# Kernel optimization log

Measured on AMD Instinct MI355X. Metric: run time of the kernel, lower is better.

The kernel has to match this reference:

```python
import jax, jax.numpy as jnp
import numpy as np

DIM = 512
LEVELS = 4
KSIZES = [3, 5, 7, 9]
NUM_HEADS = 4
GN_GROUPS = 4
GN_EPS = 1e-5
ROPE_BASE = 10000.0


def dwconv(x, w, b):
    # x: (B,C,H,W), w: (C,1,k,k) depthwise, b: (C,)
    y = jax.lax.conv_general_dilated(
        x, w, window_strides=(1, 1), padding='SAME',
        dimension_numbers=('NCHW', 'OIHW', 'NCHW'),
        feature_group_count=x.shape[1])
    return y + b[None, :, None, None]


def groupnorm(x, w, b):
    B, C, H, W = x.shape
    xg = x.reshape(B, GN_GROUPS, C // GN_GROUPS, H, W)
    mu = xg.mean(axis=(2, 3, 4), keepdims=True)
    var = xg.var(axis=(2, 3, 4), keepdims=True)
    xn = ((xg - mu) * jax.lax.rsqrt(var + GN_EPS)).reshape(B, C, H, W)
    return xn * w[None, :, None, None] + b[None, :, None, None]


def rope2d(x):
    # Faithful to the torch RoPE: rotations have shape (h, c//2) and broadcast
    # onto the trailing (w, c//2) dims of x (valid because h == w), so the
    # rotation angle effectively varies along the w axis.
    b, h, w, c = x.shape
    k_max = c // 2
    theta = 1.0 / (ROPE_BASE ** (jnp.arange(k_max, dtype=x.dtype) / k_max))
    angles = jnp.arange(h, dtype=x.dtype)[:, None] * theta[None, :]  # (h, k_max)
    cos = jnp.cos(angles)[None, None, :, :]  # broadcasts along w axis
    sin = jnp.sin(angles)[None, None, :, :]
    xp = x.reshape(b, h, w, k_max, 2)
    re, im = xp[..., 0], xp[..., 1]
    out_re = cos * re - sin * im
    out_im = cos * im + sin * re
    return jnp.stack([out_re, out_im], axis=-1).reshape(b, h, w, c)


def setup_inputs() -> dict:
    key = jax.random.key(0)
    ks = jax.random.split(key, 20)
    C = DIM
    inp = {'x': jax.random.normal(ks[0], (8, C, 64, 64), dtype=jnp.float32)}
    for i, k in enumerate(KSIZES):
        inp[f'conv_w{i}'] = jax.random.normal(ks[1 + i], (C, 1, k, k), dtype=jnp.float32) * 0.05
        inp[f'conv_b{i}'] = jnp.zeros((C,), dtype=jnp.float32)
        inp[f'gn_w{i}'] = jnp.ones((C,), dtype=jnp.float32)
        inp[f'gn_b{i}'] = jnp.zeros((C,), dtype=jnp.float32)
    inp['qk_w'] = jax.random.normal(ks[10], (2 * C, C), dtype=jnp.float32) * (C ** -0.5)
    inp['lepe_w'] = jax.random.normal(ks[11], (C, 1, 3, 3), dtype=jnp.float32) * 0.05
    inp['lepe_b'] = jnp.zeros((C,), dtype=jnp.float32)
    return inp


def reference(x, conv_w0, conv_b0, gn_w0, gn_b0, conv_w1, conv_b1, gn_w1, gn_b1,
              conv_w2, conv_b2, gn_w2, gn_b2, conv_w3, conv_b3, gn_w3, gn_b3,
              qk_w, lepe_w, lepe_b):
    conv_ws = [conv_w0, conv_w1, conv_w2, conv_w3]
    conv_bs = [conv_b0, conv_b1, conv_b2, conv_b3]
    gn_ws = [gn_w0, gn_w1, gn_w2, gn_w3]
    gn_bs = [gn_b0, gn_b1, gn_b2, gn_b3]

    # Multi-level depthwise conv -> GroupNorm -> sigmoid gate, averaged.
    fused = sum(jax.nn.sigmoid(groupnorm(dwconv(x, cw, cb), gw, gb))
                for cw, cb, gw, gb in zip(conv_ws, conv_bs, gn_ws, gn_bs)) / LEVELS

    b, c, h, w = fused.shape
    n = h * w
    H = NUM_HEADS
    hd = c // H

    tokens = fused.transpose(0, 2, 3, 1).reshape(b, n, c)  # (b, n, c)

    qk = tokens @ qk_w.T  # (b, n, 2c)
    q = jax.nn.elu(qk[..., :c]) + 1.0
    k = jax.nn.elu(qk[..., c:]) + 1.0
    v = tokens

    q_rope = rope2d(q.reshape(b, h, w, c)).reshape(b, n, H, hd).transpose(0, 2, 1, 3)
    k_rope = rope2d(k.reshape(b, h, w, c)).reshape(b, n, H, hd).transpose(0, 2, 1, 3)
    qh = q.reshape(b, n, H, hd).transpose(0, 2, 1, 3)  # (b,H,n,hd)
    kh = k.reshape(b, n, H, hd).transpose(0, 2, 1, 3)
    vh = v.reshape(b, n, H, hd).transpose(0, 2, 1, 3)

    k_mean = kh.mean(axis=2, keepdims=True)  # (b,H,1,hd)
    z = 1.0 / (jnp.einsum('bhnd,bhmd->bhnm', qh, k_mean) + 1e-6)  # (b,H,n,1)
    kv = jnp.einsum('bhnd,bhne->bhde', k_rope, vh) / n  # (b,H,hd,hd)
    attn = jnp.einsum('bhnd,bhde->bhne', q_rope, kv) * z  # (b,H,n,hd)

    out_tok = attn.transpose(0, 2, 1, 3).reshape(b, n, c)
    lepe_out = dwconv(fused, lepe_w, lepe_b)  # (b,c,h,w)
    out_tok = out_tok + lepe_out.transpose(0, 2, 3, 1).reshape(b, n, c)

    return out_tok.transpose(0, 2, 1).reshape(b, c, h, w)
```

## Files before the change

kernel.cpp:

```cpp
#include <hip/hip_runtime.h>
#include <math.h>


typedef __attribute__((ext_vector_type(8))) short bf8;
typedef __attribute__((ext_vector_type(4))) float f32x4;

__device__ __forceinline__ float waveSum(float v) {
  #pragma unroll
  for (int o = 32; o; o >>= 1) v += __shfl_down(v, o, 64);
  return v;
}

__device__ __forceinline__ unsigned short f2bf(float f) {
  unsigned u = __float_as_uint(f);
  unsigned r = u + 0x7fffu + ((u >> 16) & 1u);
  return (unsigned short)(r >> 16);
}

__device__ __forceinline__ float bf2f(unsigned short u) {
  return __uint_as_float((unsigned)u << 16);
}

__device__ __forceinline__ void gload_lds16(const void* g, void* l) {
  __builtin_amdgcn_global_load_lds(
      (const __attribute__((address_space(1))) unsigned*)g,
      (__attribute__((address_space(3))) unsigned*)l, 16, 0, 0);
}

__global__ __launch_bounds__(256) void k_ropetab(float* __restrict__ tab) {
  int idx = blockIdx.x * 256 + threadIdx.x;
  int w = idx >> 8, kk = idx & 255;
  float theta = powf(10000.0f, -(float)kk * (1.0f / 256.0f));
  float ang = (float)w * theta;
  tab[2 * idx]     = cosf(ang);
  tab[2 * idx + 1] = sinf(ang);
}

template <int K>
__device__ __forceinline__ void conv8(float (*sm)[73], const float* wl,
                                      int r, int cb, float bias, float acc[8]) {
  constexpr int P = (K - 1) / 2;
  #pragma unroll
  for (int i = 0; i < 8; i++) acc[i] = bias;
  #pragma unroll
  for (int dy = 0; dy < K; ++dy) {
    const float* row = &sm[r + dy - P + 4][cb - P + 4];
    float v[8 + K - 1];
    #pragma unroll
    for (int o = 0; o < 8 + K - 1; ++o) v[o] = row[o];
    #pragma unroll
    for (int dx = 0; dx < K; ++dx) {
      float wv = wl[dy * K + dx];
      #pragma unroll
      for (int i = 0; i < 8; i++) acc[i] = fmaf(wv, v[i + dx], acc[i]);
    }
  }
}

__device__ __forceinline__ void load_plane512(const float* __restrict__ xp,
                                              float (*sm)[73], int tid) {
  for (int idx = tid; idx < 5184; idx += 512) {
    int pr = idx / 72, pc = idx - pr * 72;
    int gr = pr - 4, gc = pc - 4;
    float v = 0.f;
    if ((unsigned)gr < 64u && (unsigned)gc < 64u) v = xp[gr * 64 + gc];
    sm[pr][pc] = v;
  }
}

__device__ __forceinline__ void load_weights512(const float* w0, const float* w1,
                                                const float* w2, const float* w3,
                                                float* wl, int c, int tid) {
  if (tid < 9)               wl[tid]            = w0[c * 9  + tid];
  else if (tid < 34)         wl[tid]            = w1[c * 25 + tid - 9];
  else if (tid < 83)         wl[tid]            = w2[c * 49 + tid - 34];
  else if (tid < 164)        wl[tid]            = w3[c * 81 + tid - 83];
}

__device__ __forceinline__ void reduce_write2_512(float s, float sq, float* red,
                                                  int tid, float* dst) {
  s = waveSum(s); sq = waveSum(sq);
  int wid = tid >> 6, lane = tid & 63;
  if (lane == 0) { red[wid] = s; red[8 + wid] = sq; }
  __syncthreads();
  if (tid == 0) {
    float S = 0.f, SQ = 0.f;
    #pragma unroll
    for (int i = 0; i < 8; i++) { S += red[i]; SQ += red[8 + i]; }
    dst[0] = S; dst[1] = SQ;
  }
  __syncthreads();
}

__global__ __launch_bounds__(512) void k_conv4(
    const float* __restrict__ x,
    const float* __restrict__ w0, const float* __restrict__ b0,
    const float* __restrict__ w1, const float* __restrict__ b1,
    const float* __restrict__ w2, const float* __restrict__ b2,
    const float* __restrict__ w3, const float* __restrict__ b3,
    float* __restrict__ part,
    unsigned short* __restrict__ l0, unsigned short* __restrict__ l1,
    unsigned short* __restrict__ l2, unsigned short* __restrict__ l3) {
  __shared__ float sm[72][73];
  __shared__ float wl[164];
  __shared__ float red[16];
  int tid = threadIdx.x;
  int bc = blockIdx.x;
  int b = bc >> 9, c = bc & 511;
  load_plane512(x + (size_t)bc * 4096, sm, tid);
  load_weights512(w0, w1, w2, w3, wl, c, tid);
  __syncthreads();
  int r = tid >> 3, cb = (tid & 7) << 3;
  size_t obase = (size_t)bc * 4096 + r * 64 + cb;
  float acc[8];
  float s, sq;
  unsigned short o[8];

  conv8<3>(sm, &wl[0], r, cb, b0[c], acc);
  s = 0; sq = 0;
  #pragma unroll
  for (int i = 0; i < 8; i++) {
    s += acc[i]; sq = fmaf(acc[i], acc[i], sq); o[i] = f2bf(acc[i]);
  }
  *(uint4*)&l0[obase] = *(uint4*)&o[0];
  reduce_write2_512(s, sq, red, tid, part + ((size_t)(0 * 8 + b) * 512 + c) * 2);
  __builtin_amdgcn_sched_barrier(0);

  conv8<5>(sm, &wl[9], r, cb, b1[c], acc);
  s = 0; sq = 0;
  #pragma unroll
  for (int i = 0; i < 8; i++) {
    s += acc[i]; sq = fmaf(acc[i], acc[i], sq); o[i] = f2bf(acc[i]);
  }
  *(uint4*)&l1[obase] = *(uint4*)&o[0];
  reduce_write2_512(s, sq, red, tid, part + ((size_t)(1 * 8 + b) * 512 + c) * 2);
  __builtin_amdgcn_sched_barrier(0);

  conv8<7>(sm, &wl[34], r, cb, b2[c], acc);
  s = 0; sq = 0;
  #pragma unroll
  for (int i = 0; i < 8; i++) {
    s += acc[i]; sq = fmaf(acc[i], acc[i], sq); o[i] = f2bf(acc[i]);
  }
  *(uint4*)&l2[obase] = *(uint4*)&o[0];
  reduce_write2_512(s, sq, red, tid, part + ((size_t)(2 * 8 + b) * 512 + c) * 2);
  __builtin_amdgcn_sched_barrier(0);

  conv8<9>(sm, &wl[83], r, cb, b3[c], acc);
  s = 0; sq = 0;
  #pragma unroll
  for (int i = 0; i < 8; i++) {
    s += acc[i]; sq = fmaf(acc[i], acc[i], sq); o[i] = f2bf(acc[i]);
  }
  *(uint4*)&l3[obase] = *(uint4*)&o[0];
  reduce_write2_512(s, sq, red, tid, part + ((size_t)(3 * 8 + b) * 512 + c) * 2);
}

__global__ __launch_bounds__(128) void k_gn_stats(const float* __restrict__ part,
                                                  float* __restrict__ stats) {
  int blk = blockIdx.x;
  int tid = threadIdx.x;
  int g = blk & 3, bb = (blk >> 2) & 7, l = blk >> 5;
  const float* p = part + ((size_t)(l * 8 + bb) * 512 + g * 128 + tid) * 2;
  float s = p[0], sq = p[1];
  s = waveSum(s); sq = waveSum(sq);
  __shared__ float red[4];
  int wid = tid >> 6, lane = tid & 63;
  if (lane == 0) { red[wid] = s; red[2 + wid] = sq; }
  __syncthreads();
  if (tid == 0) {
    float S = red[0] + red[1], SQ = red[2] + red[3];
    const float inv = 1.0f / (128.0f * 4096.0f);
    float mean = S * inv;
    float var = SQ * inv - mean * mean;
    stats[blk * 2] = mean;
    stats[blk * 2 + 1] = rsqrtf(var + 1e-5f);
  }
}

__global__ __launch_bounds__(256) void k_fused_elem(
    const unsigned short* __restrict__ l0, const unsigned short* __restrict__ l1,
    const unsigned short* __restrict__ l2, const unsigned short* __restrict__ l3,
    const float* __restrict__ gw0, const float* __restrict__ gb0,
    const float* __restrict__ gw1, const float* __restrict__ gb1,
    const float* __restrict__ gw2, const float* __restrict__ gb2,
    const float* __restrict__ gw3, const float* __restrict__ gb3,
    const float* __restrict__ stats, float* __restrict__ fused) {
  int bc = blockIdx.x;
  int b = bc >> 9, c = bc & 511, g = c >> 7;
  int tid = threadIdx.x;
  float m0 = stats[(0 * 32 + b * 4 + g) * 2], r0 = stats[(0 * 32 + b * 4 + g) * 2 + 1];
  float m1 = stats[(1 * 32 + b * 4 + g) * 2], r1 = stats[(1 * 32 + b * 4 + g) * 2 + 1];
  float m2 = stats[(2 * 32 + b * 4 + g) * 2], r2 = stats[(2 * 32 + b * 4 + g) * 2 + 1];
  float m3 = stats[(3 * 32 + b * 4 + g) * 2], r3 = stats[(3 * 32 + b * 4 + g) * 2 + 1];
  float a0 = r0 * gw0[c], c0 = gb0[c] - m0 * a0;
  float a1 = r1 * gw1[c], c1 = gb1[c] - m1 * a1;
  float a2 = r2 * gw2[c], c2 = gb2[c] - m2 * a2;
  float a3 = r3 * gw3[c], c3 = gb3[c] - m3 * a3;
  size_t base = (size_t)bc * 4096 + tid * 16;
  uint4 u0a = *(const uint4*)&l0[base], u0b = *(const uint4*)&l0[base + 8];
  uint4 u1a = *(const uint4*)&l1[base], u1b = *(const uint4*)&l1[base + 8];
  uint4 u2a = *(const uint4*)&l2[base], u2b = *(const uint4*)&l2[base + 8];
  uint4 u3a = *(const uint4*)&l3[base], u3b = *(const uint4*)&l3[base + 8];
  float outv[16];
  #pragma unroll
  for (int i = 0; i < 8; i++) {
    float t0 = fmaf(bf2f(((const unsigned short*)&u0a)[i]), a0, c0);
    float t1 = fmaf(bf2f(((const unsigned short*)&u1a)[i]), a1, c1);
    float t2 = fmaf(bf2f(((const unsigned short*)&u2a)[i]), a2, c2);
    float t3 = fmaf(bf2f(((const unsigned short*)&u3a)[i]), a3, c3);
    float s = 1.0f / (1.0f + __expf(-t0)) + 1.0f / (1.0f + __expf(-t1)) +
              1.0f / (1.0f + __expf(-t2)) + 1.0f / (1.0f + __expf(-t3));
    outv[i] = s * 0.25f;
  }
  #pragma unroll
  for (int i = 0; i < 8; i++) {
    float t0 = fmaf(bf2f(((const unsigned short*)&u0b)[i]), a0, c0);
    float t1 = fmaf(bf2f(((const unsigned short*)&u1b)[i]), a1, c1);
    float t2 = fmaf(bf2f(((const unsigned short*)&u2b)[i]), a2, c2);
    float t3 = fmaf(bf2f(((const unsigned short*)&u3b)[i]), a3, c3);
    float s = 1.0f / (1.0f + __expf(-t0)) + 1.0f / (1.0f + __expf(-t1)) +
              1.0f / (1.0f + __expf(-t2)) + 1.0f / (1.0f + __expf(-t3));
    outv[8 + i] = s * 0.25f;
  }
  float* fp = fused + base;
  #pragma unroll
  for (int i = 0; i < 16; i += 4)
    *(float4*)&fp[i] = make_float4(outv[i], outv[i + 1], outv[i + 2], outv[i + 3]);
}

__global__ __launch_bounds__(256) void k_tp(const float* __restrict__ fused,
                                            unsigned short* __restrict__ fbf) {
  __shared__ float sm[64][65];
  int tid = threadIdx.x;
  int bid = blockIdx.x;
  int nt = bid & 63, ct = (bid >> 6) & 7, b = bid >> 9;
  int c0 = ct << 6, n0 = nt << 6;
  int nn = tid & 63, c_s = tid >> 6;
  #pragma unroll
  for (int cc = 0; cc < 64; cc += 4)
    sm[cc + c_s][nn] = fused[((size_t)b * 512 + c0 + cc + c_s) * 4096 + n0 + nn];
  __syncthreads();
  int cc = tid & 63, r_s = tid >> 6;
  #pragma unroll
  for (int r = 0; r < 64; r += 4)
    fbf[((size_t)b * 4096 + n0 + r + r_s) * 512 + c0 + cc] = f2bf(sm[cc][r + r_s]);
}

__global__ __launch_bounds__(256) void k_wcvt(const float* __restrict__ qkw,
                                              unsigned short* __restrict__ wbf) {
  int gid = blockIdx.x * 256 + threadIdx.x;
  float4 v = *(const float4*)&qkw[(size_t)gid * 4];
  short4 o;
  o.x = (short)f2bf(v.x); o.y = (short)f2bf(v.y);
  o.z = (short)f2bf(v.z); o.w = (short)f2bf(v.w);
  *(short4*)&wbf[(size_t)gid * 4] = o;
}

__global__ __launch_bounds__(256) void k_qk(const unsigned short* __restrict__ fbf,
                                            const unsigned short* __restrict__ wbf,
                                            float* __restrict__ qbuf,
                                            float* __restrict__ kbuf) {
  __shared__ __align__(16) short As[8192];
  __shared__ __align__(16) short Bs[8192];
  int tid = threadIdx.x;
  int bid = blockIdx.x;
  int sw = (bid & 7) * 256 + (bid >> 3);
  int b = sw >> 8, rem = sw & 255;
  int mt_blk = rem >> 3, jt = rem & 7;
  int m0 = mt_blk << 7, j0 = jt << 7;
  int lane = tid & 63, wid = tid >> 6;
  int wm = (wid >> 1) * 64, wn = (wid & 1) * 64;
  int l15 = lane & 15, l4 = lane >> 4;

  const unsigned short* Ab = fbf + (size_t)b * 4096 * 512;
  f32x4 acc[4][4];
  #pragma unroll
  for (int i = 0; i < 4; i++)
    #pragma unroll
    for (int j = 0; j < 4; j++) acc[i][j] = (f32x4)0.f;

  int srow[4], sperm[4];
  #pragma unroll
  for (int i = 0; i < 4; i++) {
    int s = i * 256 + tid;
    srow[i] = s >> 3;
    sperm[i] = (s & 7) ^ (srow[i] & 7);
  }

  for (int t = 0; t < 8; ++t) {
    int c0 = t << 6;
    if (t) __syncthreads();
    #pragma unroll
    for (int i = 0; i < 4; i++) {
      int s = i * 256 + tid;
      gload_lds16(Ab + (size_t)(m0 + srow[i]) * 512 + c0 + sperm[i] * 8,
                  (char*)As + s * 16);
      gload_lds16(wbf + (size_t)(j0 + srow[i]) * 512 + c0 + sperm[i] * 8,
                  (char*)Bs + s * 16);
    }
    __syncthreads();
    #pragma unroll
    for (int ks = 0; ks < 2; ++ks) {
      bf8 af[4], bfr[4];
      #pragma unroll
      for (int mt = 0; mt < 4; mt++) {
        int row = wm + mt * 16 + l15;
        int g = ks * 4 + l4;
        af[mt] = *(const bf8*)((const char*)As + row * 128 + ((g ^ (row & 7)) << 4));
      }
      #pragma unroll
      for (int nt = 0; nt < 4; nt++) {
        int row = wn + nt * 16 + l15;
        int g = ks * 4 + l4;
        bfr[nt] = *(const bf8*)((const char*)Bs + row * 128 + ((g ^ (row & 7)) << 4));
      }
      #pragma unroll
      for (int mt = 0; mt < 4; mt++)
        #pragma unroll
        for (int nt = 0; nt < 4; nt++)
          acc[mt][nt] = __builtin_amdgcn_mfma_f32_16x16x32_bf16(
              af[mt], bfr[nt], acc[mt][nt], 0, 0, 0);
    }
  }

  float* dst; int jb;
  if (j0 < 512) { dst = qbuf; jb = j0; } else { dst = kbuf; jb = j0 - 512; }
  #pragma unroll
  for (int mt = 0; mt < 4; mt++) {
    #pragma unroll
    for (int nt = 0; nt < 4; nt++) {
      #pragma unroll
      for (int r = 0; r < 4; r++) {
        float v = acc[mt][nt][r];
        v = v > 0.f ? v + 1.f : __expf(v);
        int token = m0 + wm + mt * 16 + l4 * 4 + r;
        int chan = jb + wn + nt * 16 + l15;
        dst[((size_t)b * 4096 + token) * 512 + chan] = v;
      }
    }
  }
}

__global__ __launch_bounds__(256) void k_krT(const float* __restrict__ kbuf,
                                             const float* __restrict__ tab,
                                             unsigned short* __restrict__ krT,
                                             float* __restrict__ kmp) {
  __shared__ float sm[64][65];
  int tid = threadIdx.x;
  int bid = blockIdx.x;
  int nt = bid & 63, ct = (bid >> 6) & 7, b = bid >> 9;
  int c0 = ct << 6, n0 = nt << 6;
  int cc = tid & 63, n_s = tid >> 6;
  #pragma unroll
  for (int nn = 0; nn < 64; nn += 4)
    sm[cc][nn + n_s] = kbuf[((size_t)b * 4096 + n0 + nn + n_s) * 512 + c0 + cc];
  __syncthreads();
  int rc = tid >> 2, nq = tid & 3;
  int c = c0 + rc;
  int pairidx = c >> 1;
  int odd = c & 1;
  int partner = odd ? rc - 1 : rc + 1;
  unsigned short o[16];
  float colsum = 0.f;
  #pragma unroll
  for (int i = 0; i < 16; i++) {
    int nloc = nq * 16 + i;
    float2 cs = *(const float2*)&tab[2 * (nloc * 256 + pairidx)];
    float a = sm[rc][nloc], p = sm[partner][nloc];
    float r = odd ? fmaf(cs.x, a, cs.y * p) : fmaf(cs.x, a, -cs.y * p);
    o[i] = f2bf(r);
    colsum += a;
  }
  *(uint4*)&krT[((size_t)b * 512 + c) * 4096 + n0 + nq * 16]     = *(uint4*)&o[0];
  *(uint4*)&krT[((size_t)b * 512 + c) * 4096 + n0 + nq * 16 + 8] = *(uint4*)&o[8];
  colsum += __shfl_xor(colsum, 1, 64);
  colsum += __shfl_xor(colsum, 2, 64);
  if (nq == 0) kmp[((size_t)b * 64 + nt) * 512 + c] = colsum;
}

__global__ __launch_bounds__(512) void k_kmean_fin(const float* __restrict__ kmp,
                                                   float* __restrict__ kmean) {
  int b = blockIdx.x, c = threadIdx.x;
  float s = 0.f;
  for (int nt = 0; nt < 64; nt++) s += kmp[((size_t)b * 64 + nt) * 512 + c];
  kmean[b * 512 + c] = s * (1.0f / 4096.0f);
}

__global__ __launch_bounds__(256) void k_z(const float* __restrict__ qbuf,
                                           const float* __restrict__ kmean,
                                           float* __restrict__ zbuf) {
  __shared__ float kml[512];
  int blk = blockIdx.x;
  int b = blk >> 6, n0 = (blk & 63) << 6;
  int tid = threadIdx.x;
  kml[tid] = kmean[b * 512 + tid];
  kml[tid + 256] = kmean[b * 512 + 256 + tid];
  __syncthreads();
  int tt = tid >> 2, h = tid & 3;
  const float* qp = &qbuf[((size_t)b * 4096 + n0 + tt) * 512 + h * 128];
  float dot = 0.f;
  #pragma unroll
  for (int i = 0; i < 32; i++) {
    float4 qv = *(const float4*)&qp[i * 4];
    float4 kv4 = *(const float4*)&kml[h * 128 + i * 4];
    dot += qv.x * kv4.x + qv.y * kv4.y + qv.z * kv4.z + qv.w * kv4.w;
  }
  zbuf[(size_t)(b * 4 + h) * 4096 + n0 + tt] = 1.0f / (dot + 1e-6f);
}

__global__ __launch_bounds__(256) void k_kv(const unsigned short* __restrict__ krT,
                                            const float* __restrict__ fused,
                                            float* __restrict__ kvpart) {
  __shared__ __align__(16) short As[8192];
  __shared__ __align__(16) short Bs[8192];
  int tid = threadIdx.x;
  int bid = blockIdx.x;
  int bh = bid >> 3, chunk = bid & 7;
  int b = bh >> 2, h = bh & 3;
  int n_base = chunk * 512;
  int lane = tid & 63, wid = tid >> 6;
  int wm = (wid >> 1) * 64, wn = (wid & 1) * 64;
  int l15 = lane & 15, l4 = lane >> 4;

  const unsigned short* Ab = krT + ((size_t)b * 512 + h * 128) * 4096;
  const float* Vb = fused + ((size_t)b * 512 + h * 128) * 4096;
  f32x4 acc[4][4];
  #pragma unroll
  for (int i = 0; i < 4; i++)
    #pragma unroll
    for (int j = 0; j < 4; j++) acc[i][j] = (f32x4)0.f;

  int srow[4], sperm[4];
  #pragma unroll
  for (int i = 0; i < 4; i++) {
    int s = i * 256 + tid;
    srow[i] = s >> 3;
    sperm[i] = (s & 7) ^ (srow[i] & 7);
  }

  for (int t = 0; t < 8; ++t) {
    int k0 = n_base + (t << 6);
    if (t) __syncthreads();
    #pragma unroll
    for (int i = 0; i < 4; i++) {
      int s = i * 256 + tid;
      gload_lds16(Ab + (size_t)srow[i] * 4096 + k0 + sperm[i] * 8,
                  (char*)As + s * 16);
      const float* vp = &Vb[(size_t)srow[i] * 4096 + k0 + (s & 7) * 8];
      float4 v0 = *(const float4*)&vp[0];
      float4 v1 = *(const float4*)&vp[4];
      unsigned short o[8];
      o[0] = f2bf(v0.x); o[1] = f2bf(v0.y); o[2] = f2bf(v0.z); o[3] = f2bf(v0.w);
      o[4] = f2bf(v1.x); o[5] = f2bf(v1.y); o[6] = f2bf(v1.z); o[7] = f2bf(v1.w);
      *(uint4*)((char*)Bs + srow[i] * 128 + (sperm[i] << 4)) = *(uint4*)o;
    }
    __syncthreads();
    #pragma unroll
    for (int ks = 0; ks < 2; ++ks) {
      bf8 af[4], bfr[4];
      #pragma unroll
      for (int mt = 0; mt < 4; mt++) {
        int row = wm + mt * 16 + l15;
        int g = ks * 4 + l4;
        af[mt] = *(const bf8*)((const char*)As + row * 128 + ((g ^ (row & 7)) << 4));
      }
      #pragma unroll
      for (int nt = 0; nt < 4; nt++) {
        int row = wn + nt * 16 + l15;
        int g = ks * 4 + l4;
        bfr[nt] = *(const bf8*)((const char*)Bs + row * 128 + ((g ^ (row & 7)) << 4));
      }
      #pragma unroll
      for (int mt = 0; mt < 4; mt++)
        #pragma unroll
        for (int nt = 0; nt < 4; nt++)
          acc[mt][nt] = __builtin_amdgcn_mfma_f32_16x16x32_bf16(
              af[mt], bfr[nt], acc[mt][nt], 0, 0, 0);
    }
  }

  float* dst = kvpart + (size_t)(bh * 8 + chunk) * 16384;
  #pragma unroll
  for (int mt = 0; mt < 4; mt++) {
    #pragma unroll
    for (int nt = 0; nt < 4; nt++) {
      #pragma unroll
      for (int r = 0; r < 4; r++) {
        int d = wm + mt * 16 + l4 * 4 + r;
        int e = wn + nt * 16 + l15;
        dst[d * 128 + e] = acc[mt][nt][r];
      }
    }
  }
}

__global__ __launch_bounds__(256) void k_kv_fin(const float* __restrict__ part,
                                                unsigned short* __restrict__ kvT) {
  int bh = blockIdx.x;
  int tid = threadIdx.x;
  for (int idx = tid; idx < 16384; idx += 256) {
    int e = idx >> 7, d = idx & 127;
    float s = 0;
    for (int ch = 0; ch < 8; ch++)
      s += part[(size_t)(bh * 8 + ch) * 16384 + d * 128 + e];
    kvT[(size_t)bh * 16384 + idx] = f2bf(s * (1.0f / 4096.0f));
  }
}

__global__ __launch_bounds__(256) void k_lepe(const float* __restrict__ fused,
                                              const float* __restrict__ lw,
                                              const float* __restrict__ lb,
                                              float* __restrict__ out) {
  __shared__ float sm[66][67];
  __shared__ float wl[9];
  int tid = threadIdx.x;
  int bc = blockIdx.x;
  int c = bc & 511;
  const float* fp = fused + (size_t)bc * 4096;
  for (int idx = tid; idx < 4356; idx += 256) {
    int pr = idx / 66, pc = idx - pr * 66;
    int gr = pr - 1, gc = pc - 1;
    float v = 0.f;
    if ((unsigned)gr < 64u && (unsigned)gc < 64u) v = fp[gr * 64 + gc];
    sm[pr][pc] = v;
  }
  if (tid < 9) wl[tid] = lw[c * 9 + tid];
  __syncthreads();
  int r = tid >> 2, cb = (tid & 3) << 4;
  float bias = lb[c];
  float accv[16];
  #pragma unroll
  for (int i = 0; i < 16; i++) accv[i] = bias;
  #pragma unroll
  for (int dy = 0; dy < 3; dy++) {
    const float* row = &sm[r + dy][cb];
    float v[18];
    #pragma unroll
    for (int o = 0; o < 18; ++o) v[o] = row[o];
    #pragma unroll
    for (int dx = 0; dx < 3; dx++) {
      float wv = wl[dy * 3 + dx];
      #pragma unroll
      for (int i = 0; i < 16; i++) accv[i] = fmaf(wv, v[i + dx], accv[i]);
    }
  }
  float* op = out + (size_t)bc * 4096 + r * 64 + cb;
  #pragma unroll
  for (int i = 0; i < 16; i += 4)
    *(float4*)&op[i] = make_float4(accv[i], accv[i + 1], accv[i + 2], accv[i + 3]);
}

__global__ __launch_bounds__(256) void k_qrope(const float* __restrict__ qbuf,
                                               const float* __restrict__ tab,
                                               unsigned short* __restrict__ qr) {
  int gid = blockIdx.x * 256 + threadIdx.x;
  int tok = gid >> 6;
  int pg = gid & 63;
  int wpos = tok & 63;
  const float* qp = qbuf + (size_t)tok * 512 + pg * 8;
  const float* tp = tab + 2 * (wpos * 256 + pg * 4);
  float4 a  = *(const float4*)&qp[0];
  float4 b4 = *(const float4*)&qp[4];
  float4 t0 = *(const float4*)&tp[0];
  float4 t1 = *(const float4*)&tp[4];
  unsigned short o[8];
  o[0] = f2bf(t0.x * a.x - t0.y * a.y);
  o[1] = f2bf(t0.x * a.y + t0.y * a.x);
  o[2] = f2bf(t0.z * a.z - t0.w * a.w);
  o[3] = f2bf(t0.z * a.w + t0.w * a.z);
  o[4] = f2bf(t1.x * b4.x - t1.y * b4.y);
  o[5] = f2bf(t1.x * b4.y + t1.y * b4.x);
  o[6] = f2bf(t1.z * b4.z - t1.w * b4.w);
  o[7] = f2bf(t1.z * b4.w + t1.w * b4.z);
  *(uint4*)&qr[(size_t)tok * 512 + pg * 8] = *(uint4*)o;
}

__global__ __launch_bounds__(256) void k_attn(const unsigned short* __restrict__ qr,
                                              const unsigned short* __restrict__ kvT,
                                              const float* __restrict__ zbuf,
                                              float* __restrict__ out) {
  __shared__ __align__(16) short As[8192];
  __shared__ __align__(16) short Bs[8192];
  __shared__ float zl[128];
  int tid = threadIdx.x;
  int bid = blockIdx.x;
  int sw = (bid & 7) * 128 + (bid >> 3);
  int b = sw >> 7, rem = sw & 127;
  int h = rem >> 5, mt_blk = rem & 31;
  int bh = b * 4 + h;
  int m0 = mt_blk << 7;
  int lane = tid & 63, wid = tid >> 6;
  int wm = (wid >> 1) * 64, wn = (wid & 1) * 64;
  int l15 = lane & 15, l4 = lane >> 4;

  const unsigned short* Ab = qr + (size_t)b * 4096 * 512 + h * 128;
  const unsigned short* Bb = kvT + (size_t)bh * 16384;
  if (tid < 128) zl[tid] = zbuf[(size_t)bh * 4096 + m0 + tid];

  f32x4 acc[4][4];
  #pragma unroll
  for (int i = 0; i < 4; i++)
    #pragma unroll
    for (int j = 0; j < 4; j++) acc[i][j] = (f32x4)0.f;

  int srow[4], sperm[4];
  #pragma unroll
  for (int i = 0; i < 4; i++) {
    int s = i * 256 + tid;
    srow[i] = s >> 3;
    sperm[i] = (s & 7) ^ (srow[i] & 7);
  }

  for (int t = 0; t < 2; ++t) {
    int c0 = t << 6;
    if (t) __syncthreads();
    #pragma unroll
    for (int i = 0; i < 4; i++) {
      int s = i * 256 + tid;
      gload_lds16(Ab + (size_t)(m0 + srow[i]) * 512 + c0 + sperm[i] * 8,
                  (char*)As + s * 16);
      gload_lds16(Bb + srow[i] * 128 + c0 + sperm[i] * 8,
                  (char*)Bs + s * 16);
    }
    __syncthreads();
    #pragma unroll
    for (int ks = 0; ks < 2; ++ks) {
      bf8 af[4], bfr[4];
      #pragma unroll
      for (int mt = 0; mt < 4; mt++) {
        int row = wm + mt * 16 + l15;
        int g = ks * 4 + l4;
        af[mt] = *(const bf8*)((const char*)As + row * 128 + ((g ^ (row & 7)) << 4));
      }
      #pragma unroll
      for (int nt = 0; nt < 4; nt++) {
        int row = wn + nt * 16 + l15;
        int g = ks * 4 + l4;
        bfr[nt] = *(const bf8*)((const char*)Bs + row * 128 + ((g ^ (row & 7)) << 4));
      }
      #pragma unroll
      for (int mt = 0; mt < 4; mt++)
        #pragma unroll
        for (int nt = 0; nt < 4; nt++)
          acc[mt][nt] = __builtin_amdgcn_mfma_f32_16x16x32_bf16(
              af[mt], bfr[nt], acc[mt][nt], 0, 0, 0);
    }
  }

  #pragma unroll
  for (int mt = 0; mt < 4; mt++) {
    int tl = wm + mt * 16 + l4 * 4;
    float4 zv = make_float4(zl[tl], zl[tl + 1], zl[tl + 2], zl[tl + 3]);
    #pragma unroll
    for (int nt = 0; nt < 4; nt++) {
      int e = wn + nt * 16 + l15;
      float* op = &out[((size_t)b * 512 + h * 128 + e) * 4096 + m0 + tl];
      float4 o4 = *(float4*)op;
      o4.x += acc[mt][nt][0] * zv.x;
      o4.y += acc[mt][nt][1] * zv.y;
      o4.z += acc[mt][nt][2] * zv.z;
      o4.w += acc[mt][nt][3] * zv.w;
      *(float4*)op = o4;
    }
  }
}

extern "C" void kernel_launch(void* const* d_in, const int* in_sizes, int n_in,
                              void* d_out, int out_size, void* d_ws, size_t ws_size,
                              hipStream_t stream) {
  (void)in_sizes; (void)n_in; (void)out_size; (void)ws_size;
  const float* x   = (const float*)d_in[0];
  const float* cw0 = (const float*)d_in[1];
  const float* cb0 = (const float*)d_in[2];
  const float* gw0 = (const float*)d_in[3];
  const float* gb0 = (const float*)d_in[4];
  const float* cw1 = (const float*)d_in[5];
  const float* cb1 = (const float*)d_in[6];
  const float* gw1 = (const float*)d_in[7];
  const float* gb1 = (const float*)d_in[8];
  const float* cw2 = (const float*)d_in[9];
  const float* cb2 = (const float*)d_in[10];
  const float* gw2 = (const float*)d_in[11];
  const float* gb2 = (const float*)d_in[12];
  const float* cw3 = (const float*)d_in[13];
  const float* cb3 = (const float*)d_in[14];
  const float* gw3 = (const float*)d_in[15];
  const float* gb3 = (const float*)d_in[16];
  const float* qkw = (const float*)d_in[17];
  const float* lw  = (const float*)d_in[18];
  const float* lb  = (const float*)d_in[19];
  float* out = (float*)d_out;
  float* ws  = (float*)d_ws;

  float* fused    = ws;
  float* qbuf     = fused + 16777216;
  float* convpart = qbuf + 16777216;
  float* gnstats  = convpart + 32768;
  float* tab      = gnstats + 256;
  float* kmp      = tab + 32768;
  float* kmean    = kmp + 262144;
  float* zbuf     = kmean + 4096;
  float* wslot    = zbuf + 131072;
  float* regionR  = wslot + 262144;
  float* kvpart   = regionR + 8388608;
  float* kbuf     = out;
  unsigned short* lvl0    = (unsigned short*)qbuf;
  unsigned short* lvl1    = (unsigned short*)regionR;
  unsigned short* lvl2    = (unsigned short*)out;
  unsigned short* lvl3    = (unsigned short*)out + 16777216;
  unsigned short* fbf     = (unsigned short*)regionR;
  unsigned short* krT     = (unsigned short*)regionR;
  unsigned short* wbf     = (unsigned short*)wslot;
  unsigned short* kvT     = (unsigned short*)wslot;
  unsigned short* qropebf = (unsigned short*)fused;

  k_ropetab<<<dim3(64), dim3(256), 0, stream>>>(tab);
  k_conv4<<<dim3(4096), dim3(512), 0, stream>>>(
      x, cw0, cb0, cw1, cb1, cw2, cb2, cw3, cb3, convpart,
      lvl0, lvl1, lvl2, lvl3);
  k_gn_stats<<<dim3(128), dim3(128), 0, stream>>>(convpart, gnstats);
  k_fused_elem<<<dim3(4096), dim3(256), 0, stream>>>(
      lvl0, lvl1, lvl2, lvl3,
      gw0, gb0, gw1, gb1, gw2, gb2, gw3, gb3, gnstats, fused);
  k_wcvt<<<dim3(512), dim3(256), 0, stream>>>(qkw, wbf);
  k_tp<<<dim3(4096), dim3(256), 0, stream>>>(fused, fbf);
  k_qk<<<dim3(2048), dim3(256), 0, stream>>>(fbf, wbf, qbuf, kbuf);
  k_krT<<<dim3(4096), dim3(256), 0, stream>>>(kbuf, tab, krT, kmp);
  k_kmean_fin<<<dim3(8), dim3(512), 0, stream>>>(kmp, kmean);
  k_z<<<dim3(512), dim3(256), 0, stream>>>(qbuf, kmean, zbuf);
  k_kv<<<dim3(256), dim3(256), 0, stream>>>(krT, fused, kvpart);
  k_kv_fin<<<dim3(32), dim3(256), 0, stream>>>(kvpart, kvT);
  k_lepe<<<dim3(4096), dim3(256), 0, stream>>>(fused, lw, lb, out);
  k_qrope<<<dim3(8192), dim3(256), 0, stream>>>(qbuf, tab, qropebf);
  k_attn<<<dim3(1024), dim3(256), 0, stream>>>(qropebf, kvT, zbuf, out);
}
```

Measured before the change: 509.1 us.

## Fuse four-level conv into one pass; fuse GN with transpose and z with q-rope

The multi-scale depthwise conv now sweeps the 9 input rows once, loading each row with float4 reads from a padded smem plane and feeding all four kernel sizes from the same registers. The separate transpose kernel is folded into the GroupNorm/sigmoid elementwise kernel through an smem tile, and the z normalizer is computed in the same kernel that applies RoPE to q. This cuts global re-reads of fused and qbuf and removes two launches, at the cost of more live accumulators (32 floats per thread) in the conv and less parallelism in the merged z/rope kernel. The level-1 buffer moves to kvpart so it does not overlap fbf, which is now written during the same pass.

```diff
diff --git a/kernel.cpp b/kernel.cpp
--- a/kernel.cpp
+++ b/kernel.cpp
@@ -36,29 +36,8 @@
   tab[2 * idx + 1] = sinf(ang);
 }
 
-template <int K>
-__device__ __forceinline__ void conv8(float (*sm)[73], const float* wl,
-                                      int r, int cb, float bias, float acc[8]) {
-  constexpr int P = (K - 1) / 2;
-  #pragma unroll
-  for (int i = 0; i < 8; i++) acc[i] = bias;
-  #pragma unroll
-  for (int dy = 0; dy < K; ++dy) {
-    const float* row = &sm[r + dy - P + 4][cb - P + 4];
-    float v[8 + K - 1];
-    #pragma unroll
-    for (int o = 0; o < 8 + K - 1; ++o) v[o] = row[o];
-    #pragma unroll
-    for (int dx = 0; dx < K; ++dx) {
-      float wv = wl[dy * K + dx];
-      #pragma unroll
-      for (int i = 0; i < 8; i++) acc[i] = fmaf(wv, v[i + dx], acc[i]);
-    }
-  }
-}
-
 __device__ __forceinline__ void load_plane512(const float* __restrict__ xp,
-                                              float (*sm)[73], int tid) {
+                                              float (*sm)[76], int tid) {
   for (int idx = tid; idx < 5184; idx += 512) {
     int pr = idx / 72, pc = idx - pr * 72;
     int gr = pr - 4, gc = pc - 4;
@@ -71,10 +50,10 @@
 __device__ __forceinline__ void load_weights512(const float* w0, const float* w1,
                                                 const float* w2, const float* w3,
                                                 float* wl, int c, int tid) {
-  if (tid < 9)               wl[tid]            = w0[c * 9  + tid];
-  else if (tid < 34)         wl[tid]            = w1[c * 25 + tid - 9];
-  else if (tid < 83)         wl[tid]            = w2[c * 49 + tid - 34];
-  else if (tid < 164)        wl[tid]            = w3[c * 81 + tid - 83];
+  if (tid < 9)               wl[tid] = w0[c * 9  + tid];
+  else if (tid < 34)         wl[tid] = w1[c * 25 + tid - 9];
+  else if (tid < 83)         wl[tid] = w2[c * 49 + tid - 34];
+  else if (tid < 164)        wl[tid] = w3[c * 81 + tid - 83];
 }
 
 __device__ __forceinline__ void reduce_write2_512(float s, float sq, float* red,
@@ -101,7 +80,7 @@
     float* __restrict__ part,
     unsigned short* __restrict__ l0, unsigned short* __restrict__ l1,
     unsigned short* __restrict__ l2, unsigned short* __restrict__ l3) {
-  __shared__ float sm[72][73];
+  __shared__ float sm[72][76];
   __shared__ float wl[164];
   __shared__ float red[16];
   int tid = threadIdx.x;
@@ -112,46 +91,72 @@
   __syncthreads();
   int r = tid >> 3, cb = (tid & 7) << 3;
   size_t obase = (size_t)bc * 4096 + r * 64 + cb;
-  float acc[8];
+  float a0[8], a1[8], a2[8], a3[8];
+  float bi0 = b0[c], bi1 = b1[c], bi2 = b2[c], bi3 = b3[c];
+  #pragma unroll
+  for (int i = 0; i < 8; i++) { a0[i] = bi0; a1[i] = bi1; a2[i] = bi2; a3[i] = bi3; }
+
+  #pragma unroll
+  for (int dy = -4; dy <= 4; ++dy) {
+    const float* row = &sm[r + dy + 4][cb];
+    float v[16];
+    #pragma unroll
+    for (int o = 0; o < 16; o += 4)
+      *(float4*)&v[o] = *(const float4*)&row[o];
+    if (dy >= -1 && dy <= 1) {
+      #pragma unroll
+      for (int dx = -1; dx <= 1; ++dx) {
+        float wv = wl[0 + (dy + 1) * 3 + dx + 1];
+        #pragma unroll
+        for (int i = 0; i < 8; i++) a0[i] = fmaf(wv, v[i + dx + 4], a0[i]);
+      }
+    }
+    if (dy >= -2 && dy <= 2) {
+      #pragma unroll
+      for (int dx = -2; dx <= 2; ++dx) {
+        float wv = wl[9 + (dy + 2) * 5 + dx + 2];
+        #pragma unroll
+        for (int i = 0; i < 8; i++) a1[i] = fmaf(wv, v[i + dx + 4], a1[i]);
+      }
+    }
+    if (dy >= -3 && dy <= 3) {
+      #pragma unroll
+      for (int dx = -3; dx <= 3; ++dx) {
+        float wv = wl[34 + (dy + 3) * 7 + dx + 3];
+        #pragma unroll
+        for (int i = 0; i < 8; i++) a2[i] = fmaf(wv, v[i + dx + 4], a2[i]);
+      }
+    }
+    {
+      #pragma unroll
+      for (int dx = -4; dx <= 4; ++dx) {
+        float wv = wl[83 + (dy + 4) * 9 + dx + 4];
+        #pragma unroll
+        for (int i = 0; i < 8; i++) a3[i] = fmaf(wv, v[i + dx + 4], a3[i]);
+      }
+    }
+  }
+
   float s, sq;
   unsigned short o[8];
-
-  conv8<3>(sm, &wl[0], r, cb, b0[c], acc);
   s = 0; sq = 0;
   #pragma unroll
-  for (int i = 0; i < 8; i++) {
-    s += acc[i]; sq = fmaf(acc[i], acc[i], sq); o[i] = f2bf(acc[i]);
-  }
+  for (int i = 0; i < 8; i++) { s += a0[i]; sq = fmaf(a0[i], a0[i], sq); o[i] = f2bf(a0[i]); }
   *(uint4*)&l0[obase] = *(uint4*)&o[0];
   reduce_write2_512(s, sq, red, tid, part + ((size_t)(0 * 8 + b) * 512 + c) * 2);
-  __builtin_amdgcn_sched_barrier(0);
-
-  conv8<5>(sm, &wl[9], r, cb, b1[c], acc);
   s = 0; sq = 0;
   #pragma unroll
-  for (int i = 0; i < 8; i++) {
-    s += acc[i]; sq = fmaf(acc[i], acc[i], sq); o[i] = f2bf(acc[i]);
-  }
+  for (int i = 0; i < 8; i++) { s += a1[i]; sq = fmaf(a1[i], a1[i], sq); o[i] = f2bf(a1[i]); }
   *(uint4*)&l1[obase] = *(uint4*)&o[0];
   reduce_write2_512(s, sq, red, tid, part + ((size_t)(1 * 8 + b) * 512 + c) * 2);
-  __builtin_amdgcn_sched_barrier(0);
-
-  conv8<7>(sm, &wl[34], r, cb, b2[c], acc);
   s = 0; sq = 0;
   #pragma unroll
-  for (int i = 0; i < 8; i++) {
-    s += acc[i]; sq = fmaf(acc[i], acc[i], sq); o[i] = f2bf(acc[i]);
-  }
+  for (int i = 0; i < 8; i++) { s += a2[i]; sq = fmaf(a2[i], a2[i], sq); o[i] = f2bf(a2[i]); }
   *(uint4*)&l2[obase] = *(uint4*)&o[0];
   reduce_write2_512(s, sq, red, tid, part + ((size_t)(2 * 8 + b) * 512 + c) * 2);
-  __builtin_amdgcn_sched_barrier(0);
-
-  conv8<9>(sm, &wl[83], r, cb, b3[c], acc);
   s = 0; sq = 0;
   #pragma unroll
-  for (int i = 0; i < 8; i++) {
-    s += acc[i]; sq = fmaf(acc[i], acc[i], sq); o[i] = f2bf(acc[i]);
-  }
+  for (int i = 0; i < 8; i++) { s += a3[i]; sq = fmaf(a3[i], a3[i], sq); o[i] = f2bf(a3[i]); }
   *(uint4*)&l3[obase] = *(uint4*)&o[0];
   reduce_write2_512(s, sq, red, tid, part + ((size_t)(3 * 8 + b) * 512 + c) * 2);
 }
@@ -178,26 +183,31 @@
   }
 }
 
-__global__ __launch_bounds__(256) void k_fused_elem(
+__global__ __launch_bounds__(256) void k_fused_tp(
     const unsigned short* __restrict__ l0, const unsigned short* __restrict__ l1,
     const unsigned short* __restrict__ l2, const unsigned short* __restrict__ l3,
     const float* __restrict__ gw0, const float* __restrict__ gb0,
     const float* __restrict__ gw1, const float* __restrict__ gb1,
     const float* __restrict__ gw2, const float* __restrict__ gb2,
     const float* __restrict__ gw3, const float* __restrict__ gb3,
-    const float* __restrict__ stats, float* __restrict__ fused) {
-  int bc = blockIdx.x;
-  int b = bc >> 9, c = bc & 511, g = c >> 7;
-  int tid = threadIdx.x;
+    const float* __restrict__ stats, float* __restrict__ fused,
+    unsigned short* __restrict__ fbf) {
+  __shared__ float smT[64][65];
+  int tid = threadIdx.x;
+  int bid = blockIdx.x;
+  int nt = bid & 63, ct = (bid >> 6) & 7, b = bid >> 9;
+  int c0 = ct << 6, n0 = nt << 6;
+  int c_loc = tid >> 2, nq = tid & 3;
+  int c = c0 + c_loc, g = c >> 7;
   float m0 = stats[(0 * 32 + b * 4 + g) * 2], r0 = stats[(0 * 32 + b * 4 + g) * 2 + 1];
   float m1 = stats[(1 * 32 + b * 4 + g) * 2], r1 = stats[(1 * 32 + b * 4 + g) * 2 + 1];
   float m2 = stats[(2 * 32 + b * 4 + g) * 2], r2 = stats[(2 * 32 + b * 4 + g) * 2 + 1];
   float m3 = stats[(3 * 32 + b * 4 + g) * 2], r3 = stats[(3 * 32 + b * 4 + g) * 2 + 1];
-  float a0 = r0 * gw0[c], c0 = gb0[c] - m0 * a0;
-  float a1 = r1 * gw1[c], c1 = gb1[c] - m1 * a1;
-  float a2 = r2 * gw2[c], c2 = gb2[c] - m2 * a2;
-  float a3 = r3 * gw3[c], c3 = gb3[c] - m3 * a3;
-  size_t base = (size_t)bc * 4096 + tid * 16;
+  float a0 = r0 * gw0[c], c0p = gb0[c] - m0 * a0;
+  float a1 = r1 * gw1[c], c1p = gb1[c] - m1 * a1;
+  float a2 = r2 * gw2[c], c2p = gb2[c] - m2 * a2;
+  float a3 = r3 * gw3[c], c3p = gb3[c] - m3 * a3;
+  size_t base = ((size_t)b * 512 + c) * 4096 + n0 + nq * 16;
   uint4 u0a = *(const uint4*)&l0[base], u0b = *(const uint4*)&l0[base + 8];
   uint4 u1a = *(const uint4*)&l1[base], u1b = *(const uint4*)&l1[base + 8];
   uint4 u2a = *(const uint4*)&l2[base], u2b = *(const uint4*)&l2[base + 8];
@@ -205,20 +215,20 @@
   float outv[16];
   #pragma unroll
   for (int i = 0; i < 8; i++) {
-    float t0 = fmaf(bf2f(((const unsigned short*)&u0a)[i]), a0, c0);
-    float t1 = fmaf(bf2f(((const unsigned short*)&u1a)[i]), a1, c1);
-    float t2 = fmaf(bf2f(((const unsigned short*)&u2a)[i]), a2, c2);
-    float t3 = fmaf(bf2f(((const unsigned short*)&u3a)[i]), a3, c3);
+    float t0 = fmaf(bf2f(((const unsigned short*)&u0a)[i]), a0, c0p);
+    float t1 = fmaf(bf2f(((const unsigned short*)&u1a)[i]), a1, c1p);
+    float t2 = fmaf(bf2f(((const unsigned short*)&u2a)[i]), a2, c2p);
+    float t3 = fmaf(bf2f(((const unsigned short*)&u3a)[i]), a3, c3p);
     float s = 1.0f / (1.0f + __expf(-t0)) + 1.0f / (1.0f + __expf(-t1)) +
               1.0f / (1.0f + __expf(-t2)) + 1.0f / (1.0f + __expf(-t3));
     outv[i] = s * 0.25f;
   }
   #pragma unroll
   for (int i = 0; i < 8; i++) {
-    float t0 = fmaf(bf2f(((const unsigned short*)&u0b)[i]), a0, c0);
-    float t1 = fmaf(bf2f(((const unsigned short*)&u1b)[i]), a1, c1);
-    float t2 = fmaf(bf2f(((const unsigned short*)&u2b)[i]), a2, c2);
-    float t3 = fmaf(bf2f(((const unsigned short*)&u3b)[i]), a3, c3);
+    float t0 = fmaf(bf2f(((const unsigned short*)&u0b)[i]), a0, c0p);
+    float t1 = fmaf(bf2f(((const unsigned short*)&u1b)[i]), a1, c1p);
+    float t2 = fmaf(bf2f(((const unsigned short*)&u2b)[i]), a2, c2p);
+    float t3 = fmaf(bf2f(((const unsigned short*)&u3b)[i]), a3, c3p);
     float s = 1.0f / (1.0f + __expf(-t0)) + 1.0f / (1.0f + __expf(-t1)) +
               1.0f / (1.0f + __expf(-t2)) + 1.0f / (1.0f + __expf(-t3));
     outv[8 + i] = s * 0.25f;
@@ -227,24 +237,13 @@
   #pragma unroll
   for (int i = 0; i < 16; i += 4)
     *(float4*)&fp[i] = make_float4(outv[i], outv[i + 1], outv[i + 2], outv[i + 3]);
-}
-
-__global__ __launch_bounds__(256) void k_tp(const float* __restrict__ fused,
-                                            unsigned short* __restrict__ fbf) {
-  __shared__ float sm[64][65];
-  int tid = threadIdx.x;
-  int bid = blockIdx.x;
-  int nt = bid & 63, ct = (bid >> 6) & 7, b = bid >> 9;
-  int c0 = ct << 6, n0 = nt << 6;
-  int nn = tid & 63, c_s = tid >> 6;
-  #pragma unroll
-  for (int cc = 0; cc < 64; cc += 4)
-    sm[cc + c_s][nn] = fused[((size_t)b * 512 + c0 + cc + c_s) * 4096 + n0 + nn];
+  #pragma unroll
+  for (int i = 0; i < 16; i++) smT[c_loc][nq * 16 + i] = outv[i];
   __syncthreads();
   int cc = tid & 63, r_s = tid >> 6;
   #pragma unroll
-  for (int r = 0; r < 64; r += 4)
-    fbf[((size_t)b * 4096 + n0 + r + r_s) * 512 + c0 + cc] = f2bf(sm[cc][r + r_s]);
+  for (int rr = 0; rr < 64; rr += 4)
+    fbf[((size_t)b * 4096 + n0 + rr + r_s) * 512 + c0 + cc] = f2bf(smT[cc][rr + r_s]);
 }
 
 __global__ __launch_bounds__(256) void k_wcvt(const float* __restrict__ qkw,
@@ -387,9 +386,11 @@
   kmean[b * 512 + c] = s * (1.0f / 4096.0f);
 }
 
-__global__ __launch_bounds__(256) void k_z(const float* __restrict__ qbuf,
-                                           const float* __restrict__ kmean,
-                                           float* __restrict__ zbuf) {
+__global__ __launch_bounds__(256) void k_zrope(const float* __restrict__ qbuf,
+                                               const float* __restrict__ kmean,
+                                               const float* __restrict__ tab,
+                                               float* __restrict__ zbuf,
+                                               unsigned short* __restrict__ qr) {
   __shared__ float kml[512];
   int blk = blockIdx.x;
   int b = blk >> 6, n0 = (blk & 63) << 6;
@@ -399,12 +400,30 @@
   __syncthreads();
   int tt = tid >> 2, h = tid & 3;
   const float* qp = &qbuf[((size_t)b * 4096 + n0 + tt) * 512 + h * 128];
+  unsigned short* qo = &qr[((size_t)b * 4096 + n0 + tt) * 512 + h * 128];
+  const float* tp = tab + 2 * (tt * 256 + h * 64);
+  const float* km = &kml[h * 128];
   float dot = 0.f;
   #pragma unroll
-  for (int i = 0; i < 32; i++) {
-    float4 qv = *(const float4*)&qp[i * 4];
-    float4 kv4 = *(const float4*)&kml[h * 128 + i * 4];
-    dot += qv.x * kv4.x + qv.y * kv4.y + qv.z * kv4.z + qv.w * kv4.w;
+  for (int it = 0; it < 16; ++it) {
+    float4 qa = *(const float4*)&qp[it * 8];
+    float4 qb = *(const float4*)&qp[it * 8 + 4];
+    float4 ka = *(const float4*)&km[it * 8];
+    float4 kb = *(const float4*)&km[it * 8 + 4];
+    dot += qa.x * ka.x + qa.y * ka.y + qa.z * ka.z + qa.w * ka.w +
+           qb.x * kb.x + qb.y * kb.y + qb.z * kb.z + qb.w * kb.w;
+    float4 t0 = *(const float4*)&tp[it * 8];
+    float4 t1 = *(const float4*)&tp[it * 8 + 4];
+    unsigned short o[8];
+    o[0] = f2bf(t0.x * qa.x - t0.y * qa.y);
+    o[1] = f2bf(t0.x * qa.y + t0.y * qa.x);
+    o[2] = f2bf(t0.z * qa.z - t0.w * qa.w);
+    o[3] = f2bf(t0.z * qa.w + t0.w * qa.z);
+    o[4] = f2bf(t1.x * qb.x - t1.y * qb.y);
+    o[5] = f2bf(t1.x * qb.y + t1.y * qb.x);
+    o[6] = f2bf(t1.z * qb.z - t1.w * qb.w);
+    o[7] = f2bf(t1.z * qb.w + t1.w * qb.z);
+    *(uint4*)&qo[it * 8] = *(uint4*)o;
   }
   zbuf[(size_t)(b * 4 + h) * 4096 + n0 + tt] = 1.0f / (dot + 1e-6f);
 }
@@ -549,31 +568,6 @@
   #pragma unroll
   for (int i = 0; i < 16; i += 4)
     *(float4*)&op[i] = make_float4(accv[i], accv[i + 1], accv[i + 2], accv[i + 3]);
-}
-
-__global__ __launch_bounds__(256) void k_qrope(const float* __restrict__ qbuf,
-                                               const float* __restrict__ tab,
-                                               unsigned short* __restrict__ qr) {
-  int gid = blockIdx.x * 256 + threadIdx.x;
-  int tok = gid >> 6;
-  int pg = gid & 63;
-  int wpos = tok & 63;
-  const float* qp = qbuf + (size_t)tok * 512 + pg * 8;
-  const float* tp = tab + 2 * (wpos * 256 + pg * 4);
-  float4 a  = *(const float4*)&qp[0];
-  float4 b4 = *(const float4*)&qp[4];
-  float4 t0 = *(const float4*)&tp[0];
-  float4 t1 = *(const float4*)&tp[4];
-  unsigned short o[8];
-  o[0] = f2bf(t0.x * a.x - t0.y * a.y);
-  o[1] = f2bf(t0.x * a.y + t0.y * a.x);
-  o[2] = f2bf(t0.z * a.z - t0.w * a.w);
-  o[3] = f2bf(t0.z * a.w + t0.w * a.z);
-  o[4] = f2bf(t1.x * b4.x - t1.y * b4.y);
-  o[5] = f2bf(t1.x * b4.y + t1.y * b4.x);
-  o[6] = f2bf(t1.z * b4.z - t1.w * b4.w);
-  o[7] = f2bf(t1.z * b4.w + t1.w * b4.z);
-  *(uint4*)&qr[(size_t)tok * 512 + pg * 8] = *(uint4*)o;
 }
 
 __global__ __launch_bounds__(256) void k_attn(const unsigned short* __restrict__ qr,
@@ -706,7 +700,7 @@
   float* kvpart   = regionR + 8388608;
   float* kbuf     = out;
   unsigned short* lvl0    = (unsigned short*)qbuf;
-  unsigned short* lvl1    = (unsigned short*)regionR;
+  unsigned short* lvl1    = (unsigned short*)kvpart;
   unsigned short* lvl2    = (unsigned short*)out;
   unsigned short* lvl3    = (unsigned short*)out + 16777216;
   unsigned short* fbf     = (unsigned short*)regionR;
@@ -720,18 +714,16 @@
       x, cw0, cb0, cw1, cb1, cw2, cb2, cw3, cb3, convpart,
       lvl0, lvl1, lvl2, lvl3);
   k_gn_stats<<<dim3(128), dim3(128), 0, stream>>>(convpart, gnstats);
-  k_fused_elem<<<dim3(4096), dim3(256), 0, stream>>>(
+  k_fused_tp<<<dim3(4096), dim3(256), 0, stream>>>(
       lvl0, lvl1, lvl2, lvl3,
-      gw0, gb0, gw1, gb1, gw2, gb2, gw3, gb3, gnstats, fused);
+      gw0, gb0, gw1, gb1, gw2, gb2, gw3, gb3, gnstats, fused, fbf);
   k_wcvt<<<dim3(512), dim3(256), 0, stream>>>(qkw, wbf);
-  k_tp<<<dim3(4096), dim3(256), 0, stream>>>(fused, fbf);
   k_qk<<<dim3(2048), dim3(256), 0, stream>>>(fbf, wbf, qbuf, kbuf);
   k_krT<<<dim3(4096), dim3(256), 0, stream>>>(kbuf, tab, krT, kmp);
   k_kmean_fin<<<dim3(8), dim3(512), 0, stream>>>(kmp, kmean);
-  k_z<<<dim3(512), dim3(256), 0, stream>>>(qbuf, kmean, zbuf);
   k_kv<<<dim3(256), dim3(256), 0, stream>>>(krT, fused, kvpart);
   k_kv_fin<<<dim3(32), dim3(256), 0, stream>>>(kvpart, kvT);
   k_lepe<<<dim3(4096), dim3(256), 0, stream>>>(fused, lw, lb, out);
-  k_qrope<<<dim3(8192), dim3(256), 0, stream>>>(qbuf, tab, qropebf);
+  k_zrope<<<dim3(512), dim3(256), 0, stream>>>(qbuf, kmean, tab, zbuf, qropebf);
   k_attn<<<dim3(1024), dim3(256), 0, stream>>>(qropebf, kvT, zbuf, out);
 }
```

New measurement: 1.143 ms. 2.25x slower.
